# Kernel optimization log

Hardware: AMD Instinct MI355X
Metric: run time of the kernel (lower is better)

## Reference

```python
import jax, jax.numpy as jnp
import numpy as np

N = 65536        # flattened ray-sample count
K = 8            # net_kernels (experts)
WID = 64         # net_width
D = 32           # feature dim (num_output_channels)
POS_DEG = 2
VIEW_DEG = 4
DIN = D + (3 + 2 * POS_DEG * 3) + (3 + 2 * VIEW_DEG * 3)  # 74


def posenc(x, deg):
    # coord.pos_enc with min_deg=0, max_deg=deg, append_identity=True
    scales = 2.0 ** jnp.arange(deg, dtype=x.dtype)            # [deg]
    xb = (x[..., None, :] * scales[:, None]).reshape(*x.shape[:-1], deg * x.shape[-1])
    four = jnp.sin(jnp.concatenate([xb, xb + 0.5 * jnp.pi], axis=-1))
    return jnp.concatenate([x, four], axis=-1)


def multi_dense(idx, x, kernel, bias):
    # per-sample expert gather + small matmul: x [N,din], kernel [K,din,dout]
    w = kernel[idx]                                           # [N,din,dout]
    return jnp.einsum('ni,nio->no', x, w) + bias[idx]


def _he_uniform(key, shape):
    fan_in = shape[-2]
    lim = np.sqrt(6.0 / fan_in).astype(np.float32)
    return jax.random.uniform(key, shape, jnp.float32, -lim, lim)


def setup_inputs() -> dict:
    key = jax.random.key(0)
    ks = jax.random.split(key, 8)
    idxs = jax.random.randint(ks[0], (N, 1), 0, K, dtype=jnp.int32)
    positions = jax.random.normal(ks[1], (N, 3), jnp.float32)
    viewdirs = jax.random.normal(ks[2], (N, 3), jnp.float32)
    viewdirs = viewdirs / jnp.linalg.norm(viewdirs, axis=-1, keepdims=True)
    features = jax.random.normal(ks[3], (N, D), jnp.float32)
    W0 = _he_uniform(ks[4], (K, DIN, WID))
    b0 = jnp.zeros((K, WID), jnp.float32)
    W1 = _he_uniform(ks[5], (K, WID, WID))
    b1 = jnp.zeros((K, WID), jnp.float32)
    W2 = _he_uniform(ks[6], (K, WID, D))
    b2 = jnp.zeros((K, D), jnp.float32)
    return {'idxs': idxs, 'positions': positions, 'viewdirs': viewdirs,
            'features': features, 'W0': W0, 'b0': b0, 'W1': W1, 'b1': b1,
            'W2': W2, 'b2': b2}


def reference(idxs, positions, viewdirs, features, W0, b0, W1, b1, W2, b2):
    idx = idxs.reshape(-1)                                    # [N]
    x = jnp.concatenate([features,
                         posenc(positions, POS_DEG),
                         posenc(viewdirs, VIEW_DEG)], axis=-1)  # [N, DIN]
    h = jax.nn.relu(multi_dense(idx, x, W0, b0))              # [N, WID]
    h = jax.nn.relu(multi_dense(idx, h, W1, b1))              # [N, WID]
    return multi_dense(idx, h, W2, b2)                        # [N, D]
```

## Files before the change

kernel.cpp:

```cpp
#include <hip/hip_runtime.h>
#include <hip/hip_bf16.h>

#define NS    65536
#define KEXP  8
#define WID   64
#define DOUT  32
#define DIN   74
#define TM    64
#define XS    104
#define HS    72
#define GX    64
#define NB    64

typedef __attribute__((ext_vector_type(8))) short short8;
typedef __attribute__((ext_vector_type(4))) float floatx4;

__device__ __forceinline__ unsigned short f2b(float f) {
  unsigned u = __builtin_bit_cast(unsigned, f);
  u = u + 0x7FFFu + ((u >> 16) & 1u);
  return (unsigned short)(u >> 16);
}


__global__ __launch_bounds__(1024) void k_scatter(const int* __restrict__ idxs,
                                                  unsigned short* __restrict__ bucket,
                                                  int* __restrict__ hist) {
  __shared__ int lc[KEXP];
  const int tid = threadIdx.x;
  const int b = blockIdx.x;
  if (tid < KEXP) lc[tid] = 0;
  __syncthreads();
  const int gid = b * 1024 + tid;
  const int e = idxs[gid];
  const int rank = atomicAdd(&lc[e], 1);
  bucket[(e << 16) + (b << 10) + rank] = (unsigned short)gid;
  __syncthreads();
  if (tid < KEXP) hist[b * KEXP + tid] = lc[tid];
}

__device__ __forceinline__ int seg_search(unsigned p, unsigned c, int pp, int* lcl) {
  int lo = 0, hi = NB - 1;
#pragma unroll
  for (int it = 0; it < 6; ++it) {
    const int mid = (lo + hi) >> 1;
    const unsigned pm = (unsigned)__shfl((int)p, mid, 64);
    if (pm > (unsigned)pp) hi = mid;
    else lo = mid + 1;
  }
  const unsigned base = (unsigned)__shfl((int)(p - c), lo, 64);
  *lcl = pp - (int)base;
  return lo;
}

__global__ __launch_bounds__(256, 3) void k_mlp(
    const int* __restrict__ hist,
    const unsigned short* __restrict__ bucket,
    const float* __restrict__ pos,
    const float* __restrict__ view,
    const float* __restrict__ feat,
    const float* __restrict__ W0,
    const float* __restrict__ B0,
    const float* __restrict__ W1,
    const float* __restrict__ B1,
    const float* __restrict__ W2,
    const float* __restrict__ B2,
    float* __restrict__ out)
{
  const int e = blockIdx.y;
  const int tid = threadIdx.x;
  const int lane = tid & 63;
  const int wv = tid >> 6;
  const int quad = lane >> 4;
  const int r16 = lane & 15;
  const int rb = wv * 16;

  __shared__ __align__(16) unsigned short Xs[TM * XS];
  __shared__ __align__(16) unsigned short W0t[WID * XS];
  __shared__ __align__(16) unsigned short W1t[WID * HS];
  __shared__ __align__(16) unsigned short W2t[DOUT * HS];
  __shared__ __align__(16) unsigned short Hs[TM * HS];
  __shared__ float sb0[WID];
  __shared__ float sb1[WID];
  __shared__ float sb2[DOUT];
  __shared__ int sid[TM];

  const unsigned c = (unsigned)hist[lane * KEXP + e];
  unsigned p = c;
#pragma unroll
  for (int st = 1; st < NB; st <<= 1) {
    const unsigned v = __shfl_up(p, st, 64);
    if (lane >= st) p += v;
  }
  const int segCnt = __shfl((int)p, NB - 1, 64);
  if ((int)blockIdx.x * TM >= segCnt) return;

  int s_pre = 0;
  float4 fA, fB, fC, fD;

  auto gather = [&](int t0, int rows) {
    const int pp = t0 + min(lane, rows - 1);
    int local;
    const int sb_ = seg_search(p, c, pp, &local);
    if (lane < rows) {
      s_pre = (int)bucket[(e << 16) + (sb_ << 10) + local];
      if (wv == 0) {
        const float4* fs = (const float4*)(feat + (size_t)s_pre * DOUT);
        fA = fs[0]; fB = fs[1]; fC = fs[2]; fD = fs[3];
      } else if (wv == 1) {
        const float4* fs = (const float4*)(feat + (size_t)s_pre * DOUT);
        fA = fs[4]; fB = fs[5]; fC = fs[6]; fD = fs[7];
      } else if (wv == 2) {
        fA.x = pos[s_pre * 3 + 0];
        fA.y = pos[s_pre * 3 + 1];
        fA.z = pos[s_pre * 3 + 2];
      } else {
        fA.x = view[s_pre * 3 + 0];
        fA.y = view[s_pre * 3 + 1];
        fA.z = view[s_pre * 3 + 2];
      }
    }
  };

  {
    const int t0 = (int)blockIdx.x * TM;
    gather(t0, min(TM, segCnt - t0));
  }

  for (int i = tid; i < TM * XS; i += 256) Xs[i] = 0;
  for (int g = tid; g < WID * 7; g += 256) {
    const int o = g / 7, ch = g % 7;
    *(uint2*)&W0t[o * XS + 76 + ch * 4] = make_uint2(0u, 0u);
  }

  {
    const float* g0 = W0 + (size_t)e * DIN * WID;
    for (int g = tid; g < 19 * WID; g += 256) {
      const int o = g & 63, i4 = g >> 6, ib = i4 * 4;
      unsigned v0 = 0, v1 = 0;
#pragma unroll
      for (int j = 0; j < 4; ++j) {
        const int i = ib + j;
        unsigned short w = (i < DIN) ? f2b(g0[i * WID + o]) : (unsigned short)0;
        if (j < 2) v0 |= (unsigned)w << (16 * j);
        else       v1 |= (unsigned)w << (16 * (j - 2));
      }
      *(uint2*)&W0t[o * XS + ib] = make_uint2(v0, v1);
    }
    const float* g1 = W1 + (size_t)e * WID * WID;
    for (int g = tid; g < 16 * WID; g += 256) {
      const int o = g & 63, i4 = g >> 6, ib = i4 * 4;
      unsigned v0, v1;
      v0 = (unsigned)f2b(g1[(ib + 0) * WID + o]) | ((unsigned)f2b(g1[(ib + 1) * WID + o]) << 16);
      v1 = (unsigned)f2b(g1[(ib + 2) * WID + o]) | ((unsigned)f2b(g1[(ib + 3) * WID + o]) << 16);
      *(uint2*)&W1t[o * HS + ib] = make_uint2(v0, v1);
    }
    const float* g2 = W2 + (size_t)e * WID * DOUT;
    for (int g = tid; g < 16 * DOUT; g += 256) {
      const int o = g & 31, i4 = g >> 5, ib = i4 * 4;
      unsigned v0, v1;
      v0 = (unsigned)f2b(g2[(ib + 0) * DOUT + o]) | ((unsigned)f2b(g2[(ib + 1) * DOUT + o]) << 16);
      v1 = (unsigned)f2b(g2[(ib + 2) * DOUT + o]) | ((unsigned)f2b(g2[(ib + 3) * DOUT + o]) << 16);
      *(uint2*)&W2t[o * HS + ib] = make_uint2(v0, v1);
    }
    if (tid < WID) {
      sb0[tid] = B0[e * WID + tid];
      sb1[tid] = B1[e * WID + tid];
    } else if (tid < WID + DOUT) {
      const int t = tid - WID;
      sb2[t] = B2[e * DOUT + t];
    }
  }
  __syncthreads();

  for (int tile = blockIdx.x; tile * TM < segCnt; tile += GX) {
    const int t0 = tile * TM;
    const int rows = min(TM, segCnt - t0);

    if (tile != (int)blockIdx.x) {
      __syncthreads();
    }

    if (lane < rows) {
      unsigned short* xr = &Xs[lane * XS];
      if (wv == 0) {
        sid[lane] = s_pre;
        xr[0]  = f2b(fA.x); xr[1]  = f2b(fA.y); xr[2]  = f2b(fA.z); xr[3]  = f2b(fA.w);
        xr[4]  = f2b(fB.x); xr[5]  = f2b(fB.y); xr[6]  = f2b(fB.z); xr[7]  = f2b(fB.w);
        xr[8]  = f2b(fC.x); xr[9]  = f2b(fC.y); xr[10] = f2b(fC.z); xr[11] = f2b(fC.w);
        xr[12] = f2b(fD.x); xr[13] = f2b(fD.y); xr[14] = f2b(fD.z); xr[15] = f2b(fD.w);
      } else if (wv == 1) {
        xr[16] = f2b(fA.x); xr[17] = f2b(fA.y); xr[18] = f2b(fA.z); xr[19] = f2b(fA.w);
        xr[20] = f2b(fB.x); xr[21] = f2b(fB.y); xr[22] = f2b(fB.z); xr[23] = f2b(fB.w);
        xr[24] = f2b(fC.x); xr[25] = f2b(fC.y); xr[26] = f2b(fC.z); xr[27] = f2b(fC.w);
        xr[28] = f2b(fD.x); xr[29] = f2b(fD.y); xr[30] = f2b(fD.z); xr[31] = f2b(fD.w);
      } else if (wv == 2) {
        float p3[3] = {fA.x, fA.y, fA.z};
#pragma unroll
        for (int d = 0; d < 3; ++d) xr[32 + d] = f2b(p3[d]);
#pragma unroll
        for (int si = 0; si < 2; ++si) {
          const float sc = (float)(1 << si);
#pragma unroll
          for (int d = 0; d < 3; ++d) {
            const float a = p3[d] * sc;
            xr[35 + si * 3 + d] = f2b(__sinf(a));
            xr[41 + si * 3 + d] = f2b(__cosf(a));
          }
        }
      } else {
        float v3[3] = {fA.x, fA.y, fA.z};
#pragma unroll
        for (int d = 0; d < 3; ++d) xr[47 + d] = f2b(v3[d]);
#pragma unroll
        for (int si = 0; si < 4; ++si) {
          const float sc = (float)(1 << si);
#pragma unroll
          for (int d = 0; d < 3; ++d) {
            const float a = v3[d] * sc;
            xr[50 + si * 3 + d] = f2b(__sinf(a));
            xr[62 + si * 3 + d] = f2b(__cosf(a));
          }
        }
      }
    }
    __syncthreads();

    {
      const int nt0 = t0 + GX * TM;
      if (nt0 < segCnt) gather(nt0, min(TM, segCnt - nt0));
    }

    {
      const short8 a0 = *(const short8*)&Xs[(rb + r16) * XS + 0 + quad * 8];
      const short8 a1 = *(const short8*)&Xs[(rb + r16) * XS + 32 + quad * 8];
      const short8 a2 = *(const short8*)&Xs[(rb + r16) * XS + 64 + quad * 8];
#pragma unroll
      for (int cc = 0; cc < 4; ++cc) {
        const int n0 = cc * 16;
        floatx4 acc = {0.f, 0.f, 0.f, 0.f};
        acc = __builtin_amdgcn_mfma_f32_16x16x32_bf16(
            a0, *(const short8*)&W0t[(n0 + r16) * XS + 0 + quad * 8], acc, 0, 0, 0);
        acc = __builtin_amdgcn_mfma_f32_16x16x32_bf16(
            a1, *(const short8*)&W0t[(n0 + r16) * XS + 32 + quad * 8], acc, 0, 0, 0);
        acc = __builtin_amdgcn_mfma_f32_16x16x32_bf16(
            a2, *(const short8*)&W0t[(n0 + r16) * XS + 64 + quad * 8], acc, 0, 0, 0);
        const float bias = sb0[n0 + r16];
#pragma unroll
        for (int g = 0; g < 4; ++g) {
          const float vv = fmaxf(acc[g] + bias, 0.f);
          Hs[(rb + quad * 4 + g) * HS + n0 + r16] = f2b(vv);
        }
      }
    }

    {
      const short8 h0 = *(const short8*)&Hs[(rb + r16) * HS + 0 + quad * 8];
      const short8 h1 = *(const short8*)&Hs[(rb + r16) * HS + 32 + quad * 8];
#pragma unroll
      for (int cc = 0; cc < 4; ++cc) {
        const int n0 = cc * 16;
        floatx4 acc = {0.f, 0.f, 0.f, 0.f};
        acc = __builtin_amdgcn_mfma_f32_16x16x32_bf16(
            h0, *(const short8*)&W1t[(n0 + r16) * HS + 0 + quad * 8], acc, 0, 0, 0);
        acc = __builtin_amdgcn_mfma_f32_16x16x32_bf16(
            h1, *(const short8*)&W1t[(n0 + r16) * HS + 32 + quad * 8], acc, 0, 0, 0);
        const float bias = sb1[n0 + r16];
#pragma unroll
        for (int g = 0; g < 4; ++g) {
          const float vv = fmaxf(acc[g] + bias, 0.f);
          Hs[(rb + quad * 4 + g) * HS + n0 + r16] = f2b(vv);
        }
      }
    }

    {
      const short8 q0 = *(const short8*)&Hs[(rb + r16) * HS + 0 + quad * 8];
      const short8 q1 = *(const short8*)&Hs[(rb + r16) * HS + 32 + quad * 8];
#pragma unroll
      for (int cc = 0; cc < 2; ++cc) {
        const int n0 = cc * 16;
        floatx4 acc = {0.f, 0.f, 0.f, 0.f};
        acc = __builtin_amdgcn_mfma_f32_16x16x32_bf16(
            q0, *(const short8*)&W2t[(n0 + r16) * HS + 0 + quad * 8], acc, 0, 0, 0);
        acc = __builtin_amdgcn_mfma_f32_16x16x32_bf16(
            q1, *(const short8*)&W2t[(n0 + r16) * HS + 32 + quad * 8], acc, 0, 0, 0);
        const float bias = sb2[n0 + r16];
        const int col = n0 + r16;
#pragma unroll
        for (int g = 0; g < 4; ++g) {
          const int row = rb + quad * 4 + g;
          if (row < rows) {
            out[(size_t)sid[row] * DOUT + col] = acc[g] + bias;
          }
        }
      }
    }
  }
}

extern "C" void kernel_launch(void* const* d_in, const int* in_sizes, int n_in,
                              void* d_out, int out_size, void* d_ws, size_t ws_size,
                              hipStream_t stream) {
  const int* idxs        = (const int*)d_in[0];
  const float* pos       = (const float*)d_in[1];
  const float* view      = (const float*)d_in[2];
  const float* feat      = (const float*)d_in[3];
  const float* W0        = (const float*)d_in[4];
  const float* b0        = (const float*)d_in[5];
  const float* W1        = (const float*)d_in[6];
  const float* b1        = (const float*)d_in[7];
  const float* W2        = (const float*)d_in[8];
  const float* b2        = (const float*)d_in[9];
  float* out             = (float*)d_out;
  unsigned short* bucket = (unsigned short*)d_ws;
  int* hist              = (int*)((char*)d_ws + (size_t)KEXP * NB * 1024 * 2);

  k_scatter<<<NB, 1024, 0, stream>>>(idxs, bucket, hist);
  dim3 grid(GX, KEXP);
  k_mlp<<<grid, 256, 0, stream>>>(hist, bucket, pos, view, feat,
                                  W0, b0, W1, b1, W2, b2, out);
}
```

Measured before the change: 101.0 us.

## Fuse expert bucketing and MLP into one cooperative kernel with grid sync

```diff
diff --git a/kernel.cpp b/kernel.cpp
--- a/kernel.cpp
+++ b/kernel.cpp
@@ -1,4 +1,5 @@
 #include <hip/hip_runtime.h>
+#include <hip/hip_cooperative_groups.h>
 #include <hip/hip_bf16.h>
 
 #define NS    65536
@@ -10,7 +11,10 @@
 #define XS    104
 #define HS    72
 #define GX    64
-#define NB    64
+#define NBC   128
+#define CHS   512
+
+namespace cg = cooperative_groups;
 
 typedef __attribute__((ext_vector_type(8))) short short8;
 typedef __attribute__((ext_vector_type(4))) float floatx4;
@@ -22,39 +26,10 @@
 }
 
 
-__global__ __launch_bounds__(1024) void k_scatter(const int* __restrict__ idxs,
-                                                  unsigned short* __restrict__ bucket,
-                                                  int* __restrict__ hist) {
-  __shared__ int lc[KEXP];
-  const int tid = threadIdx.x;
-  const int b = blockIdx.x;
-  if (tid < KEXP) lc[tid] = 0;
-  __syncthreads();
-  const int gid = b * 1024 + tid;
-  const int e = idxs[gid];
-  const int rank = atomicAdd(&lc[e], 1);
-  bucket[(e << 16) + (b << 10) + rank] = (unsigned short)gid;
-  __syncthreads();
-  if (tid < KEXP) hist[b * KEXP + tid] = lc[tid];
-}
-
-__device__ __forceinline__ int seg_search(unsigned p, unsigned c, int pp, int* lcl) {
-  int lo = 0, hi = NB - 1;
-#pragma unroll
-  for (int it = 0; it < 6; ++it) {
-    const int mid = (lo + hi) >> 1;
-    const unsigned pm = (unsigned)__shfl((int)p, mid, 64);
-    if (pm > (unsigned)pp) hi = mid;
-    else lo = mid + 1;
-  }
-  const unsigned base = (unsigned)__shfl((int)(p - c), lo, 64);
-  *lcl = pp - (int)base;
-  return lo;
-}
-
-__global__ __launch_bounds__(256, 3) void k_mlp(
-    const int* __restrict__ hist,
-    const unsigned short* __restrict__ bucket,
+__global__ __launch_bounds__(256, 2) void k_fused(
+    int* __restrict__ hist,
+    unsigned short* __restrict__ bucket,
+    const int* __restrict__ idxs,
     const float* __restrict__ pos,
     const float* __restrict__ view,
     const float* __restrict__ feat,
@@ -73,6 +48,7 @@
   const int quad = lane >> 4;
   const int r16 = lane & 15;
   const int rb = wv * 16;
+  const int flat = e * GX + (int)blockIdx.x;
 
   __shared__ __align__(16) unsigned short Xs[TM * XS];
   __shared__ __align__(16) unsigned short W0t[WID * XS];
@@ -83,15 +59,78 @@
   __shared__ float sb1[WID];
   __shared__ float sb2[DOUT];
   __shared__ int sid[TM];
-
-  const unsigned c = (unsigned)hist[lane * KEXP + e];
-  unsigned p = c;
-#pragma unroll
-  for (int st = 1; st < NB; st <<= 1) {
-    const unsigned v = __shfl_up(p, st, 64);
-    if (lane >= st) p += v;
-  }
-  const int segCnt = __shfl((int)p, NB - 1, 64);
+  __shared__ int lc[KEXP];
+
+  if (flat < NBC) {
+    if (tid < KEXP) lc[tid] = 0;
+    __syncthreads();
+    const int base = flat * CHS;
+    const int2 ii = *(const int2*)&idxs[base + tid * 2];
+    const int r0 = atomicAdd(&lc[ii.x], 1);
+    bucket[(ii.x << 16) + (flat << 9) + r0] = (unsigned short)(base + tid * 2);
+    const int r1 = atomicAdd(&lc[ii.y], 1);
+    bucket[(ii.y << 16) + (flat << 9) + r1] = (unsigned short)(base + tid * 2 + 1);
+    __syncthreads();
+    if (tid < KEXP) hist[tid * NBC + flat] = lc[tid];
+    __threadfence();
+  }
+
+  for (int i = tid; i < TM * XS; i += 256) Xs[i] = 0;
+  for (int g = tid; g < WID * 7; g += 256) {
+    const int o = g / 7, ch = g % 7;
+    *(uint2*)&W0t[o * XS + 76 + ch * 4] = make_uint2(0u, 0u);
+  }
+  {
+    const float* g0 = W0 + (size_t)e * DIN * WID;
+    for (int g = tid; g < 19 * WID; g += 256) {
+      const int o = g & 63, i4 = g >> 6, ib = i4 * 4;
+      unsigned v0 = 0, v1 = 0;
+#pragma unroll
+      for (int j = 0; j < 4; ++j) {
+        const int i = ib + j;
+        unsigned short w = (i < DIN) ? f2b(g0[i * WID + o]) : (unsigned short)0;
+        if (j < 2) v0 |= (unsigned)w << (16 * j);
+        else       v1 |= (unsigned)w << (16 * (j - 2));
+      }
+      *(uint2*)&W0t[o * XS + ib] = make_uint2(v0, v1);
+    }
+    const float* g1 = W1 + (size_t)e * WID * WID;
+    for (int g = tid; g < 16 * WID; g += 256) {
+      const int o = g & 63, i4 = g >> 6, ib = i4 * 4;
+      unsigned v0, v1;
+      v0 = (unsigned)f2b(g1[(ib + 0) * WID + o]) | ((unsigned)f2b(g1[(ib + 1) * WID + o]) << 16);
+      v1 = (unsigned)f2b(g1[(ib + 2) * WID + o]) | ((unsigned)f2b(g1[(ib + 3) * WID + o]) << 16);
+      *(uint2*)&W1t[o * HS + ib] = make_uint2(v0, v1);
+    }
+    const float* g2 = W2 + (size_t)e * WID * DOUT;
+    for (int g = tid; g < 16 * DOUT; g += 256) {
+      const int o = g & 31, i4 = g >> 5, ib = i4 * 4;
+      unsigned v0, v1;
+      v0 = (unsigned)f2b(g2[(ib + 0) * DOUT + o]) | ((unsigned)f2b(g2[(ib + 1) * DOUT + o]) << 16);
+      v1 = (unsigned)f2b(g2[(ib + 2) * DOUT + o]) | ((unsigned)f2b(g2[(ib + 3) * DOUT + o]) << 16);
+      *(uint2*)&W2t[o * HS + ib] = make_uint2(v0, v1);
+    }
+    if (tid < WID) {
+      sb0[tid] = B0[e * WID + tid];
+      sb1[tid] = B1[e * WID + tid];
+    } else if (tid < WID + DOUT) {
+      const int t = tid - WID;
+      sb2[t] = B2[e * DOUT + t];
+    }
+  }
+
+  cg::this_grid().sync();
+
+  const int2 cc = *(const int2*)&hist[e * NBC + lane * 2];
+  const unsigned s0 = (unsigned)cc.x;
+  const unsigned Tt = (unsigned)(cc.x + cc.y);
+  unsigned pincl = Tt;
+#pragma unroll
+  for (int st = 1; st < 64; st <<= 1) {
+    const unsigned v = __shfl_up(pincl, st, 64);
+    if (lane >= st) pincl += v;
+  }
+  const int segCnt = __shfl((int)pincl, 63, 64);
   if ((int)blockIdx.x * TM >= segCnt) return;
 
   int s_pre = 0;
@@ -99,10 +138,23 @@
 
   auto gather = [&](int t0, int rows) {
     const int pp = t0 + min(lane, rows - 1);
-    int local;
-    const int sb_ = seg_search(p, c, pp, &local);
+    int lo = 0, hi = 63;
+#pragma unroll
+    for (int it = 0; it < 6; ++it) {
+      const int mid = (lo + hi) >> 1;
+      const unsigned pm = (unsigned)__shfl((int)pincl, mid, 64);
+      if (pm > (unsigned)pp) hi = mid;
+      else lo = mid + 1;
+    }
+    const unsigned p_lo  = (unsigned)__shfl((int)pincl, lo, 64);
+    const unsigned T_lo  = (unsigned)__shfl((int)Tt, lo, 64);
+    const unsigned s0_lo = (unsigned)__shfl((int)s0, lo, 64);
+    const unsigned E_lo  = p_lo - T_lo;
+    int chunk, local;
+    if (E_lo + s0_lo > (unsigned)pp) { chunk = lo * 2;     local = pp - (int)E_lo; }
+    else                             { chunk = lo * 2 + 1; local = pp - (int)(E_lo + s0_lo); }
     if (lane < rows) {
-      s_pre = (int)bucket[(e << 16) + (sb_ << 10) + local];
+      s_pre = (int)bucket[(e << 16) + (chunk << 9) + local];
       if (wv == 0) {
         const float4* fs = (const float4*)(feat + (size_t)s_pre * DOUT);
         fA = fs[0]; fB = fs[1]; fC = fs[2]; fD = fs[3];
@@ -125,52 +177,6 @@
     const int t0 = (int)blockIdx.x * TM;
     gather(t0, min(TM, segCnt - t0));
   }
-
-  for (int i = tid; i < TM * XS; i += 256) Xs[i] = 0;
-  for (int g = tid; g < WID * 7; g += 256) {
-    const int o = g / 7, ch = g % 7;
-    *(uint2*)&W0t[o * XS + 76 + ch * 4] = make_uint2(0u, 0u);
-  }
-
-  {
-    const float* g0 = W0 + (size_t)e * DIN * WID;
-    for (int g = tid; g < 19 * WID; g += 256) {
-      const int o = g & 63, i4 = g >> 6, ib = i4 * 4;
-      unsigned v0 = 0, v1 = 0;
-#pragma unroll
-      for (int j = 0; j < 4; ++j) {
-        const int i = ib + j;
-        unsigned short w = (i < DIN) ? f2b(g0[i * WID + o]) : (unsigned short)0;
-        if (j < 2) v0 |= (unsigned)w << (16 * j);
-        else       v1 |= (unsigned)w << (16 * (j - 2));
-      }
-      *(uint2*)&W0t[o * XS + ib] = make_uint2(v0, v1);
-    }
-    const float* g1 = W1 + (size_t)e * WID * WID;
-    for (int g = tid; g < 16 * WID; g += 256) {
-      const int o = g & 63, i4 = g >> 6, ib = i4 * 4;
-      unsigned v0, v1;
-      v0 = (unsigned)f2b(g1[(ib + 0) * WID + o]) | ((unsigned)f2b(g1[(ib + 1) * WID + o]) << 16);
-      v1 = (unsigned)f2b(g1[(ib + 2) * WID + o]) | ((unsigned)f2b(g1[(ib + 3) * WID + o]) << 16);
-      *(uint2*)&W1t[o * HS + ib] = make_uint2(v0, v1);
-    }
-    const float* g2 = W2 + (size_t)e * WID * DOUT;
-    for (int g = tid; g < 16 * DOUT; g += 256) {
-      const int o = g & 31, i4 = g >> 5, ib = i4 * 4;
-      unsigned v0, v1;
-      v0 = (unsigned)f2b(g2[(ib + 0) * DOUT + o]) | ((unsigned)f2b(g2[(ib + 1) * DOUT + o]) << 16);
-      v1 = (unsigned)f2b(g2[(ib + 2) * DOUT + o]) | ((unsigned)f2b(g2[(ib + 3) * DOUT + o]) << 16);
-      *(uint2*)&W2t[o * HS + ib] = make_uint2(v0, v1);
-    }
-    if (tid < WID) {
-      sb0[tid] = B0[e * WID + tid];
-      sb1[tid] = B1[e * WID + tid];
-    } else if (tid < WID + DOUT) {
-      const int t = tid - WID;
-      sb2[t] = B2[e * DOUT + t];
-    }
-  }
-  __syncthreads();
 
   for (int tile = blockIdx.x; tile * TM < segCnt; tile += GX) {
     const int t0 = tile * TM;
@@ -235,8 +241,8 @@
       const short8 a1 = *(const short8*)&Xs[(rb + r16) * XS + 32 + quad * 8];
       const short8 a2 = *(const short8*)&Xs[(rb + r16) * XS + 64 + quad * 8];
 #pragma unroll
-      for (int cc = 0; cc < 4; ++cc) {
-        const int n0 = cc * 16;
+      for (int ccn = 0; ccn < 4; ++ccn) {
+        const int n0 = ccn * 16;
         floatx4 acc = {0.f, 0.f, 0.f, 0.f};
         acc = __builtin_amdgcn_mfma_f32_16x16x32_bf16(
             a0, *(const short8*)&W0t[(n0 + r16) * XS + 0 + quad * 8], acc, 0, 0, 0);
@@ -257,8 +263,8 @@
       const short8 h0 = *(const short8*)&Hs[(rb + r16) * HS + 0 + quad * 8];
       const short8 h1 = *(const short8*)&Hs[(rb + r16) * HS + 32 + quad * 8];
 #pragma unroll
-      for (int cc = 0; cc < 4; ++cc) {
-        const int n0 = cc * 16;
+      for (int ccn = 0; ccn < 4; ++ccn) {
+        const int n0 = ccn * 16;
         floatx4 acc = {0.f, 0.f, 0.f, 0.f};
         acc = __builtin_amdgcn_mfma_f32_16x16x32_bf16(
             h0, *(const short8*)&W1t[(n0 + r16) * HS + 0 + quad * 8], acc, 0, 0, 0);
@@ -277,8 +283,8 @@
       const short8 q0 = *(const short8*)&Hs[(rb + r16) * HS + 0 + quad * 8];
       const short8 q1 = *(const short8*)&Hs[(rb + r16) * HS + 32 + quad * 8];
 #pragma unroll
-      for (int cc = 0; cc < 2; ++cc) {
-        const int n0 = cc * 16;
+      for (int ccn = 0; ccn < 2; ++ccn) {
+        const int n0 = ccn * 16;
         floatx4 acc = {0.f, 0.f, 0.f, 0.f};
         acc = __builtin_amdgcn_mfma_f32_16x16x32_bf16(
             q0, *(const short8*)&W2t[(n0 + r16) * HS + 0 + quad * 8], acc, 0, 0, 0);
@@ -301,22 +307,23 @@
 extern "C" void kernel_launch(void* const* d_in, const int* in_sizes, int n_in,
                               void* d_out, int out_size, void* d_ws, size_t ws_size,
                               hipStream_t stream) {
-  const int* idxs        = (const int*)d_in[0];
-  const float* pos       = (const float*)d_in[1];
-  const float* view      = (const float*)d_in[2];
-  const float* feat      = (const float*)d_in[3];
-  const float* W0        = (const float*)d_in[4];
-  const float* b0        = (const float*)d_in[5];
-  const float* W1        = (const float*)d_in[6];
-  const float* b1        = (const float*)d_in[7];
-  const float* W2        = (const float*)d_in[8];
-  const float* b2        = (const float*)d_in[9];
-  float* out             = (float*)d_out;
+  const int* idxs   = (const int*)d_in[0];
+  const float* pos  = (const float*)d_in[1];
+  const float* view = (const float*)d_in[2];
+  const float* feat = (const float*)d_in[3];
+  const float* W0   = (const float*)d_in[4];
+  const float* b0   = (const float*)d_in[5];
+  const float* W1   = (const float*)d_in[6];
+  const float* b1   = (const float*)d_in[7];
+  const float* W2   = (const float*)d_in[8];
+  const float* b2   = (const float*)d_in[9];
+  float* out        = (float*)d_out;
   unsigned short* bucket = (unsigned short*)d_ws;
-  int* hist              = (int*)((char*)d_ws + (size_t)KEXP * NB * 1024 * 2);
-
-  k_scatter<<<NB, 1024, 0, stream>>>(idxs, bucket, hist);
-  dim3 grid(GX, KEXP);
-  k_mlp<<<grid, 256, 0, stream>>>(hist, bucket, pos, view, feat,
-                                  W0, b0, W1, b1, W2, b2, out);
+  int* hist = (int*)((char*)d_ws + (size_t)KEXP * NBC * CHS * 2);
+
+  dim3 grid(GX, KEXP), blk(256, 1, 1);
+  void* args[] = {(void*)&hist, (void*)&bucket, (void*)&idxs, (void*)&pos,
+                  (void*)&view, (void*)&feat, (void*)&W0, (void*)&b0,
+                  (void*)&W1, (void*)&b1, (void*)&W2, (void*)&b2, (void*)&out};
+  hipLaunchCooperativeKernel((const void*)k_fused, grid, blk, args, 0, stream);
 }
```

Result: slower. 172.3 us (+70.5%).
